# Performance work log

Hardware: AMD Instinct MI355X
Metric: run time of the kernel (lower is better)

## Reference

```python
import jax, jax.numpy as jnp
import numpy as np

EMBED = 1024
HEADS = 16
HEAD_DIM = EMBED // HEADS


def setup_inputs() -> dict:
    key = jax.random.key(0)
    k1, k2, k3 = jax.random.split(key, 3)
    B, T = 4, 2048
    query = jax.random.normal(k1, (B, T, EMBED), dtype=jnp.float32)
    # xavier-ish scaled weights
    in_proj_w = jax.random.normal(k2, (3 * EMBED, EMBED), dtype=jnp.float32) * (1.0 / np.sqrt(EMBED))
    in_proj_b = jnp.zeros((3 * EMBED,), dtype=jnp.float32)
    out_proj_w = jax.random.normal(k3, (EMBED, EMBED), dtype=jnp.float32) * (1.0 / np.sqrt(EMBED))
    out_proj_b = jnp.zeros((EMBED,), dtype=jnp.float32)
    return {"query": query, "in_proj_w": in_proj_w, "in_proj_b": in_proj_b,
            "out_proj_w": out_proj_w, "out_proj_b": out_proj_b}


def reference(query, in_proj_w, in_proj_b, out_proj_w, out_proj_b):
    # Self-attention (qkv_same path), batch_first=True, dropout=0 (eval).
    B, T, E = query.shape
    H, D = HEADS, HEAD_DIM
    scaling = D ** -0.5
    # fused QKV projection: [B,T,3E]
    qkv = jnp.einsum('bte,fe->btf', query, in_proj_w) + in_proj_b
    q, k, v = jnp.split(qkv, 3, axis=-1)
    q = q * scaling
    # reshape to [B,H,T,D]
    q = q.reshape(B, T, H, D).transpose(0, 2, 1, 3)
    k = k.reshape(B, T, H, D).transpose(0, 2, 1, 3)
    v = v.reshape(B, T, H, D).transpose(0, 2, 1, 3)
    scores = jnp.einsum('bhqd,bhkd->bhqk', q, k)
    attn = jax.nn.softmax(scores, axis=-1)
    ctx = jnp.einsum('bhqk,bhkd->bhqd', attn, v)  # [B,H,T,D]
    ctx = ctx.transpose(0, 2, 1, 3).reshape(B, T, E)
    out = jnp.einsum('bte,fe->btf', ctx, out_proj_w) + out_proj_b
    return out
```

## Files before the change

### kernel.cpp

```cpp
#include <hip/hip_runtime.h>
#include <math.h>

using bf16x8 = __attribute__((ext_vector_type(8))) short;
using f32x4  = __attribute__((ext_vector_type(4))) float;
using u16x8  = __attribute__((ext_vector_type(8))) unsigned short;
using u16x4  = __attribute__((ext_vector_type(4))) unsigned short;

constexpr int Bb = 4, Tt = 2048, Ee = 1024, Hh = 16;
constexpr int Mm = Bb * Tt;
constexpr int E3 = 3 * Ee;

__device__ __forceinline__ unsigned short f2bf(float f) {
  union { float f; unsigned int u; } c; c.f = f;
  unsigned int u = c.u;
  u += 0x7fffu + ((u >> 16) & 1u);
  return (unsigned short)(u >> 16);
}

__device__ __forceinline__ f32x4 mfma16(bf16x8 a, bf16x8 b, f32x4 c) {
  return __builtin_amdgcn_mfma_f32_16x16x32_bf16(a, b, c, 0, 0, 0);
}

__device__ __forceinline__ void gload_lds16(const unsigned short* g, unsigned short* l) {
  __builtin_amdgcn_global_load_lds(
      (const __attribute__((address_space(1))) unsigned int*)g,
      (__attribute__((address_space(3))) unsigned int*)l, 16, 0, 0);
}

__global__ void cvt_all(const float* __restrict__ q, const float* __restrict__ iw,
                        const float* __restrict__ ow, unsigned short* __restrict__ qb,
                        unsigned short* __restrict__ wib, unsigned short* __restrict__ wob) {
  constexpr int nQ = Mm * Ee / 8, nI = E3 * Ee / 8, nO = Ee * Ee / 8;
  int i = blockIdx.x * 256 + threadIdx.x;
  const float* in; unsigned short* out;
  if (i < nQ) { in = q; out = qb; }
  else if (i < nQ + nI) { in = iw; out = wib; i -= nQ; }
  else if (i < nQ + nI + nO) { in = ow; out = wob; i -= nQ + nI; }
  else return;
  const float4* p = (const float4*)in + (size_t)i * 2;
  const float4 a = p[0], b = p[1];
  u16x8 r = { f2bf(a.x), f2bf(a.y), f2bf(a.z), f2bf(a.w),
              f2bf(b.x), f2bf(b.y), f2bf(b.z), f2bf(b.w) };
  *(u16x8*)(out + (size_t)i * 8) = r;
}

template <bool OUT_BF16, bool QSCALE>
__global__ __launch_bounds__(256, 2)
void gemm_bt(const unsigned short* __restrict__ A, const unsigned short* __restrict__ Bw,
             const float* __restrict__ bias, void* __restrict__ Cout, int N, int K) {
  __shared__ alignas(16) unsigned short As[128 * 32];
  __shared__ alignas(16) unsigned short Bs[128 * 32];
  const int tid = threadIdx.x;
  const int wave = tid >> 6, lane = tid & 63;
  const int l15 = lane & 15, quad = lane >> 4;
  const int wr = wave >> 1, wc = wave & 1;
  const int row0 = blockIdx.y * 128, col0 = blockIdx.x * 128;
  const int srow = lane >> 2, sslot = lane & 3;

  f32x4 acc[4][4];
#pragma unroll
  for (int i = 0; i < 4; ++i)
#pragma unroll
    for (int j = 0; j < 4; ++j) acc[i][j] = f32x4{0.f, 0.f, 0.f, 0.f};

  for (int k0 = 0; k0 < K; k0 += 32) {
#pragma unroll
    for (int t = 0; t < 2; ++t) {
      const int rA = wave * 32 + t * 16 + srow;
      const int g = sslot ^ ((rA >> 1) & 3);
      gload_lds16(A  + (size_t)(row0 + rA) * K + k0 + g * 8, &As[(wave * 32 + t * 16) * 32]);
      gload_lds16(Bw + (size_t)(col0 + rA) * K + k0 + g * 8, &Bs[(wave * 32 + t * 16) * 32]);
    }
    __syncthreads();

    bf16x8 af[4], bfr[4];
#pragma unroll
    for (int mi = 0; mi < 4; ++mi) {
      const int m = wr * 64 + mi * 16 + l15;
      af[mi] = *(const bf16x8*)&As[m * 32 + (quad ^ ((m >> 1) & 3)) * 8];
    }
#pragma unroll
    for (int ni = 0; ni < 4; ++ni) {
      const int n = wc * 64 + ni * 16 + l15;
      bfr[ni] = *(const bf16x8*)&Bs[n * 32 + (quad ^ ((n >> 1) & 3)) * 8];
    }
#pragma unroll
    for (int mi = 0; mi < 4; ++mi)
#pragma unroll
      for (int ni = 0; ni < 4; ++ni) acc[mi][ni] = mfma16(af[mi], bfr[ni], acc[mi][ni]);
    __syncthreads();
  }

#pragma unroll
  for (int mi = 0; mi < 4; ++mi)
#pragma unroll
    for (int ni = 0; ni < 4; ++ni) {
      const int col = col0 + wc * 64 + ni * 16 + l15;
      const float bv = bias[col];
      const float scale = (QSCALE && col < 1024) ? 0.18033688f : 1.0f;
#pragma unroll
      for (int r = 0; r < 4; ++r) {
        const int row = row0 + wr * 64 + mi * 16 + quad * 4 + r;
        float v = (acc[mi][ni][r] + bv) * scale;
        if (OUT_BF16)
          ((unsigned short*)Cout)[(size_t)row * N + col] = f2bf(v);
        else
          ((float*)Cout)[(size_t)row * N + col] = v;
      }
    }
}

__global__ __launch_bounds__(256, 2)
void transpose_v(const unsigned short* __restrict__ qkv, unsigned short* __restrict__ vt) {
  __shared__ unsigned short L[128][66];
  const int tid = threadIdx.x;
  const int bh = blockIdx.x, b = bh >> 4, h = bh & 15;
  const int t0 = blockIdx.y * 128;
#pragma unroll
  for (int p = 0; p < 8; ++p) {
    const int tl = p * 16 + (tid >> 4);
    const int d = (tid & 15) * 4;
    *(u16x4*)&L[tl][d] = *(const u16x4*)(qkv + (size_t)(b * Tt + t0 + tl) * E3 + 2 * Ee + h * 64 + d);
  }
  __syncthreads();
#pragma unroll
  for (int p = 0; p < 8; ++p) {
    const int dw = (tid >> 5) * 8 + p;
    const int tw = (tid & 31) * 4;
    u16x4 w = { L[tw][dw], L[tw + 1][dw], L[tw + 2][dw], L[tw + 3][dw] };
    *(u16x4*)(vt + ((size_t)bh * 64 + dw) * Tt + t0 + tw) = w;
  }
}

__global__ __launch_bounds__(256, 2)
void attn_mfma6(const unsigned short* __restrict__ qkv,
                const unsigned short* __restrict__ vt,
                unsigned short* __restrict__ ctx) {
  __shared__ alignas(16) unsigned short Ps[4 * 4096];
  const int tid = threadIdx.x;
  const int wave = tid >> 6, lane = tid & 63;
  const int l15 = lane & 15, quad = lane >> 4;
  const int bh = blockIdx.x, b = bh >> 4, h = bh & 15;
  const int q0 = blockIdx.y * 256 + wave * 64;
  unsigned short* const ps = &Ps[wave * 4096];
  const int swz = l15 & 14;

  bf16x8 qa[4][2];
#pragma unroll
  for (int qi = 0; qi < 4; ++qi)
#pragma unroll
    for (int kf = 0; kf < 2; ++kf)
      qa[qi][kf] = *(const bf16x8*)(qkv +
          (size_t)(b * Tt + q0 + qi * 16 + l15) * E3 + h * 64 + kf * 32 + quad * 8);

  f32x4 o[4][4], ol[4];
#pragma unroll
  for (int qi = 0; qi < 4; ++qi) {
    ol[qi] = f32x4{0.f, 0.f, 0.f, 0.f};
#pragma unroll
    for (int di = 0; di < 4; ++di) o[qi][di] = f32x4{0.f, 0.f, 0.f, 0.f};
  }
  bf16x8 ones;
#pragma unroll
  for (int i = 0; i < 8; ++i) ones[i] = (short)0x3F80;

  const unsigned short* kp = qkv + (size_t)(b * Tt + l15) * E3 + Ee + h * 64 + quad * 8;
  const unsigned short* vp = vt + ((size_t)bh * 64 + l15) * Tt + quad * 8;

  bf16x8 kb[4][2], vb[4][2];
#pragma unroll
  for (int ki = 0; ki < 4; ++ki)
#pragma unroll
    for (int kf = 0; kf < 2; ++kf)
      kb[ki][kf] = *(const bf16x8*)(kp + (size_t)ki * 16 * E3 + kf * 32);
#pragma unroll
  for (int di = 0; di < 4; ++di)
#pragma unroll
    for (int kf = 0; kf < 2; ++kf)
      vb[di][kf] = *(const bf16x8*)(vp + di * 16 * Tt + kf * 32);
  kp += 64 * E3;
  vp += 64;

  f32x4 sp[4], sn[4];

  auto expwrite = [&](int slot) __attribute__((always_inline)) {
#pragma unroll
    for (int qi = 0; qi < 4; ++qi) {
      const float e0 = __builtin_amdgcn_exp2f(sp[qi][0]);
      const float e1 = __builtin_amdgcn_exp2f(sp[qi][1]);
      const float e2 = __builtin_amdgcn_exp2f(sp[qi][2]);
      const float e3 = __builtin_amdgcn_exp2f(sp[qi][3]);
      uint2 w;
      w.x = __builtin_amdgcn_perm(__float_as_uint(e1), __float_as_uint(e0), 0x07060302u);
      w.y = __builtin_amdgcn_perm(__float_as_uint(e3), __float_as_uint(e2), 0x07060302u);
      *(uint2*)(ps + (qi * 16 + l15) * 64 + (((slot * 4 + quad) ^ swz) << 2)) = w;
    }
  };
  auto Sstep = [&](int ki) __attribute__((always_inline)) {
#pragma unroll
    for (int qi = 0; qi < 4; ++qi) {
      sn[qi] = mfma16(kb[ki][0], qa[qi][0], f32x4{0.f, 0.f, 0.f, 0.f});
      sn[qi] = mfma16(kb[ki][1], qa[qi][1], sn[qi]);
    }
  };
  auto copy_sp = [&]() __attribute__((always_inline)) {
#pragma unroll
    for (int qi = 0; qi < 4; ++qi) sp[qi] = sn[qi];
  };
  auto pvstep = [&](bool reload_vb) __attribute__((always_inline)) {
#pragma unroll
    for (int qi = 0; qi < 4; ++qi) {
      bf16x8 pa0 = *(const bf16x8*)(ps + (qi * 16 + l15) * 64 + (((quad * 2) ^ swz) << 2));
      bf16x8 pa1 = *(const bf16x8*)(ps + (qi * 16 + l15) * 64 + (((8 + quad * 2) ^ swz) << 2));
      ol[qi] = mfma16(pa0, ones, ol[qi]);
      ol[qi] = mfma16(pa1, ones, ol[qi]);
#pragma unroll
      for (int di = 0; di < 4; ++di) {
        o[qi][di] = mfma16(pa0, vb[di][0], o[qi][di]);
        o[qi][di] = mfma16(pa1, vb[di][1], o[qi][di]);
      }
    }
    if (reload_vb) {
#pragma unroll
      for (int di = 0; di < 4; ++di)
#pragma unroll
        for (int kf = 0; kf < 2; ++kf)
          vb[di][kf] = *(const bf16x8*)(vp + di * 16 * Tt + kf * 32);
      vp += 64;
    }
  };

  Sstep(0); copy_sp();
  kb[0][0] = *(const bf16x8*)(kp);
  kb[0][1] = *(const bf16x8*)(kp + 32);

  for (int j = 0; j < 31; ++j) {
    expwrite(0);
    Sstep(1);
    kb[1][0] = *(const bf16x8*)(kp + (size_t)16 * E3);
    kb[1][1] = *(const bf16x8*)(kp + (size_t)16 * E3 + 32);
    copy_sp();
    expwrite(1);
    Sstep(2);
    kb[2][0] = *(const bf16x8*)(kp + (size_t)32 * E3);
    kb[2][1] = *(const bf16x8*)(kp + (size_t)32 * E3 + 32);
    copy_sp();
    expwrite(2);
    Sstep(3);
    kb[3][0] = *(const bf16x8*)(kp + (size_t)48 * E3);
    kb[3][1] = *(const bf16x8*)(kp + (size_t)48 * E3 + 32);
    kp += 64 * E3;
    copy_sp();
    expwrite(3);
    Sstep(0);
    if (j < 30) {
      kb[0][0] = *(const bf16x8*)(kp);
      kb[0][1] = *(const bf16x8*)(kp + 32);
    }
    copy_sp();
    pvstep(true);
  }
  expwrite(0); Sstep(1); copy_sp();
  expwrite(1); Sstep(2); copy_sp();
  expwrite(2); Sstep(3); copy_sp();
  expwrite(3);
  pvstep(false);

#pragma unroll
  for (int qi = 0; qi < 4; ++qi) {
    f32x4 inv;
#pragma unroll
    for (int r = 0; r < 4; ++r) inv[r] = 1.0f / ol[qi][r];
#pragma unroll
    for (int di = 0; di < 4; ++di)
#pragma unroll
      for (int r = 0; r < 4; ++r)
        ctx[(size_t)(b * Tt + q0 + qi * 16 + quad * 4 + r) * Ee + h * 64 + di * 16 + l15] =
            f2bf(o[qi][di][r] * inv[r]);
  }
}

extern "C" void kernel_launch(void* const* d_in, const int* in_sizes, int n_in,
                              void* d_out, int out_size, void* d_ws, size_t ws_size,
                              hipStream_t stream) {
  const float* query = (const float*)d_in[0];
  const float* in_w  = (const float*)d_in[1];
  const float* in_b  = (const float*)d_in[2];
  const float* out_w = (const float*)d_in[3];
  const float* out_b = (const float*)d_in[4];
  float* out = (float*)d_out;

  char* w = (char*)d_ws;
  unsigned short* qkvb = (unsigned short*)(w);
  unsigned short* ctxb = (unsigned short*)(w + 50331648);
  unsigned short* qb   = (unsigned short*)(w + 67108864);
  unsigned short* wib  = (unsigned short*)(w + 83886080);
  unsigned short* wob  = (unsigned short*)(w + 90177536);
  unsigned short* vtb  = (unsigned short*)(w + 92274688);

  cvt_all<<<6144, 256, 0, stream>>>(query, in_w, out_w, qb, wib, wob);
  gemm_bt<true, true><<<dim3(E3 / 128, Mm / 128), 256, 0, stream>>>(qb, wib, in_b, qkvb, E3, Ee);
  transpose_v<<<dim3(Bb * Hh, Tt / 128), 256, 0, stream>>>(qkvb, vtb);
  attn_mfma6<<<dim3(Bb * Hh, Tt / 256), 256, 0, stream>>>(qkvb, vtb, ctxb);
  gemm_bt<false, false><<<dim3(Ee / 128, Mm / 128), 256, 0, stream>>>(ctxb, wob, out_b, out, Ee, Ee);
}
```

Before: 313.0 us.

## Split attention key range across wave pairs and merge partial sums in LDS

Doubles the attention block to 512 threads so that each 64-query group is handled by two waves. Each wave processes half of the key sequence, so each wave runs half as many loop iterations. The second wave writes its partial output and row-sum to LDS, and the first wave adds them before normalizing and storing. This aims to raise the number of waves per CU and shorten each wave's serial loop. The costs are doubled LDS, an extra combine step with two barriers, and a tighter per-thread register budget under the new launch bounds, which could cause spills.

```diff
diff --git a/kernel.cpp b/kernel.cpp
--- a/kernel.cpp
+++ b/kernel.cpp
@@ -132,16 +132,18 @@
   }
 }
 
-__global__ __launch_bounds__(256, 2)
+__global__ __launch_bounds__(512, 2)
 void attn_mfma6(const unsigned short* __restrict__ qkv,
                 const unsigned short* __restrict__ vt,
                 unsigned short* __restrict__ ctx) {
-  __shared__ alignas(16) unsigned short Ps[4 * 4096];
+  __shared__ alignas(16) unsigned short Ps[8 * 4096];
+  __shared__ float olpart[4][64];
   const int tid = threadIdx.x;
   const int wave = tid >> 6, lane = tid & 63;
   const int l15 = lane & 15, quad = lane >> 4;
+  const int qgroup = wave >> 1, khalf = wave & 1;
   const int bh = blockIdx.x, b = bh >> 4, h = bh & 15;
-  const int q0 = blockIdx.y * 256 + wave * 64;
+  const int q0 = blockIdx.y * 256 + qgroup * 64;
   unsigned short* const ps = &Ps[wave * 4096];
   const int swz = l15 & 14;
 
@@ -164,8 +166,8 @@
 #pragma unroll
   for (int i = 0; i < 8; ++i) ones[i] = (short)0x3F80;
 
-  const unsigned short* kp = qkv + (size_t)(b * Tt + l15) * E3 + Ee + h * 64 + quad * 8;
-  const unsigned short* vp = vt + ((size_t)bh * 64 + l15) * Tt + quad * 8;
+  const unsigned short* kp = qkv + (size_t)(b * Tt + khalf * 1024 + l15) * E3 + Ee + h * 64 + quad * 8;
+  const unsigned short* vp = vt + ((size_t)bh * 64 + l15) * Tt + khalf * 1024 + quad * 8;
 
   bf16x8 kb[4][2], vb[4][2];
 #pragma unroll
@@ -234,7 +236,7 @@
   kb[0][0] = *(const bf16x8*)(kp);
   kb[0][1] = *(const bf16x8*)(kp + 32);
 
-  for (int j = 0; j < 31; ++j) {
+  for (int j = 0; j < 15; ++j) {
     expwrite(0);
     Sstep(1);
     kb[1][0] = *(const bf16x8*)(kp + (size_t)16 * E3);
@@ -253,7 +255,7 @@
     copy_sp();
     expwrite(3);
     Sstep(0);
-    if (j < 30) {
+    if (j < 14) {
       kb[0][0] = *(const bf16x8*)(kp);
       kb[0][1] = *(const bf16x8*)(kp + 32);
     }
@@ -266,17 +268,40 @@
   expwrite(3);
   pvstep(false);
 
-#pragma unroll
-  for (int qi = 0; qi < 4; ++qi) {
-    f32x4 inv;
-#pragma unroll
-    for (int r = 0; r < 4; ++r) inv[r] = 1.0f / ol[qi][r];
-#pragma unroll
-    for (int di = 0; di < 4; ++di)
+  __syncthreads();
+  float* const po = (float*)&Ps[(size_t)qgroup * 8192];
+  if (khalf) {
+#pragma unroll
+    for (int qi = 0; qi < 4; ++qi)
+#pragma unroll
+      for (int di = 0; di < 4; ++di)
+#pragma unroll
+        for (int r = 0; r < 4; ++r)
+          po[((qi * 4 + di) * 4 + r) * 64 + lane] = o[qi][di][r];
+    if (l15 == 0)
+#pragma unroll
+      for (int qi = 0; qi < 4; ++qi)
+#pragma unroll
+        for (int r = 0; r < 4; ++r)
+          olpart[qgroup][qi * 16 + quad * 4 + r] = ol[qi][r];
+  }
+  __syncthreads();
+  if (!khalf) {
+#pragma unroll
+    for (int qi = 0; qi < 4; ++qi) {
+      f32x4 inv;
 #pragma unroll
       for (int r = 0; r < 4; ++r)
-        ctx[(size_t)(b * Tt + q0 + qi * 16 + quad * 4 + r) * Ee + h * 64 + di * 16 + l15] =
-            f2bf(o[qi][di][r] * inv[r]);
+        inv[r] = 1.0f / (ol[qi][r] + olpart[qgroup][qi * 16 + quad * 4 + r]);
+#pragma unroll
+      for (int di = 0; di < 4; ++di)
+#pragma unroll
+        for (int r = 0; r < 4; ++r) {
+          const float v = o[qi][di][r] + po[((qi * 4 + di) * 4 + r) * 64 + lane];
+          ctx[(size_t)(b * Tt + q0 + qi * 16 + quad * 4 + r) * Ee + h * 64 + di * 16 + l15] =
+              f2bf(v * inv[r]);
+        }
+    }
   }
 }
 
@@ -301,6 +326,6 @@
   cvt_all<<<6144, 256, 0, stream>>>(query, in_w, out_w, qb, wib, wob);
   gemm_bt<true, true><<<dim3(E3 / 128, Mm / 128), 256, 0, stream>>>(qb, wib, in_b, qkvb, E3, Ee);
   transpose_v<<<dim3(Bb * Hh, Tt / 128), 256, 0, stream>>>(qkvb, vtb);
-  attn_mfma6<<<dim3(Bb * Hh, Tt / 256), 256, 0, stream>>>(qkvb, vtb, ctxb);
+  attn_mfma6<<<dim3(Bb * Hh, Tt / 256), 512, 0, stream>>>(qkvb, vtb, ctxb);
   gemm_bt<false, false><<<dim3(Ee / 128, Mm / 128), 256, 0, stream>>>(ctxb, wob, out_b, out, Ee, Ee);
 }
```

Result: slower. 319.6 us (+2.1%).

## Fuse V transpose into QKV GEMM epilogue and raise priority during PV MFMAs

Applied to the files above, without the earlier changes.

The QKV projection GEMM now writes the V slice directly in transposed [B,H,D,T] layout through an LDS staging tile, so the separate transpose_v kernel and its re-read of V from global memory are removed. V columns are no longer written to the qkv buffer, since attention reads V only from the transposed buffer. The attention kernel also raises wave priority around the PV MFMA block with s_setprio to favour the matrix pipe. The cost is extra LDS and two block-wide barriers in the GEMM epilogue for the V-tile blocks.

```diff
diff --git a/kernel.cpp b/kernel.cpp
--- a/kernel.cpp
+++ b/kernel.cpp
@@ -44,10 +44,11 @@
   *(u16x8*)(out + (size_t)i * 8) = r;
 }
 
-template <bool OUT_BF16, bool QSCALE>
+template <bool OUT_BF16, bool QSCALE, bool VT>
 __global__ __launch_bounds__(256, 2)
 void gemm_bt(const unsigned short* __restrict__ A, const unsigned short* __restrict__ Bw,
-             const float* __restrict__ bias, void* __restrict__ Cout, int N, int K) {
+             const float* __restrict__ bias, void* __restrict__ Cout,
+             unsigned short* __restrict__ vt, int N, int K) {
   __shared__ alignas(16) unsigned short As[128 * 32];
   __shared__ alignas(16) unsigned short Bs[128 * 32];
   const int tid = threadIdx.x;
@@ -91,6 +92,41 @@
     __syncthreads();
   }
 
+  if constexpr (VT) {
+    if (col0 >= 2048) {
+      __shared__ unsigned short Ct[64][136];
+      const int b  = row0 >> 11;
+      const int t0 = row0 & 2047;
+#pragma unroll
+      for (int hh = 0; hh < 2; ++hh) {
+        __syncthreads();
+        if (wc == hh) {
+#pragma unroll
+          for (int ni = 0; ni < 4; ++ni) {
+            const int d = ni * 16 + l15;
+            const float bv = bias[col0 + hh * 64 + d];
+#pragma unroll
+            for (int mi = 0; mi < 4; ++mi) {
+              const int t = wr * 64 + mi * 16 + quad * 4;
+              u16x4 wv;
+#pragma unroll
+              for (int r = 0; r < 4; ++r) wv[r] = f2bf(acc[mi][ni][r] + bv);
+              *(u16x4*)&Ct[d][t] = wv;
+            }
+          }
+        }
+        __syncthreads();
+        const int d = tid >> 2, tq = (tid & 3) * 32;
+        const int bh = b * 16 + ((col0 - 2048) >> 6) + hh;
+#pragma unroll
+        for (int s = 0; s < 4; ++s)
+          *(u16x8*)(vt + ((size_t)bh * 64 + d) * (size_t)Tt + t0 + tq + s * 8) =
+              *(const u16x8*)&Ct[d][tq + s * 8];
+      }
+      return;
+    }
+  }
+
 #pragma unroll
   for (int mi = 0; mi < 4; ++mi)
 #pragma unroll
@@ -108,28 +144,6 @@
           ((float*)Cout)[(size_t)row * N + col] = v;
       }
     }
-}
-
-__global__ __launch_bounds__(256, 2)
-void transpose_v(const unsigned short* __restrict__ qkv, unsigned short* __restrict__ vt) {
-  __shared__ unsigned short L[128][66];
-  const int tid = threadIdx.x;
-  const int bh = blockIdx.x, b = bh >> 4, h = bh & 15;
-  const int t0 = blockIdx.y * 128;
-#pragma unroll
-  for (int p = 0; p < 8; ++p) {
-    const int tl = p * 16 + (tid >> 4);
-    const int d = (tid & 15) * 4;
-    *(u16x4*)&L[tl][d] = *(const u16x4*)(qkv + (size_t)(b * Tt + t0 + tl) * E3 + 2 * Ee + h * 64 + d);
-  }
-  __syncthreads();
-#pragma unroll
-  for (int p = 0; p < 8; ++p) {
-    const int dw = (tid >> 5) * 8 + p;
-    const int tw = (tid & 31) * 4;
-    u16x4 w = { L[tw][dw], L[tw + 1][dw], L[tw + 2][dw], L[tw + 3][dw] };
-    *(u16x4*)(vt + ((size_t)bh * 64 + dw) * Tt + t0 + tw) = w;
-  }
 }
 
 __global__ __launch_bounds__(256, 2)
@@ -208,6 +222,7 @@
     for (int qi = 0; qi < 4; ++qi) sp[qi] = sn[qi];
   };
   auto pvstep = [&](bool reload_vb) __attribute__((always_inline)) {
+    __builtin_amdgcn_s_setprio(1);
 #pragma unroll
     for (int qi = 0; qi < 4; ++qi) {
       bf16x8 pa0 = *(const bf16x8*)(ps + (qi * 16 + l15) * 64 + (((quad * 2) ^ swz) << 2));
@@ -220,6 +235,7 @@
         o[qi][di] = mfma16(pa1, vb[di][1], o[qi][di]);
       }
     }
+    __builtin_amdgcn_s_setprio(0);
     if (reload_vb) {
 #pragma unroll
       for (int di = 0; di < 4; ++di)
@@ -299,8 +315,9 @@
   unsigned short* vtb  = (unsigned short*)(w + 92274688);
 
   cvt_all<<<6144, 256, 0, stream>>>(query, in_w, out_w, qb, wib, wob);
-  gemm_bt<true, true><<<dim3(E3 / 128, Mm / 128), 256, 0, stream>>>(qb, wib, in_b, qkvb, E3, Ee);
-  transpose_v<<<dim3(Bb * Hh, Tt / 128), 256, 0, stream>>>(qkvb, vtb);
+  gemm_bt<true, true, true><<<dim3(E3 / 128, Mm / 128), 256, 0, stream>>>(
+      qb, wib, in_b, qkvb, vtb, E3, Ee);
   attn_mfma6<<<dim3(Bb * Hh, Tt / 256), 256, 0, stream>>>(qkvb, vtb, ctxb);
-  gemm_bt<false, false><<<dim3(Ee / 128, Mm / 128), 256, 0, stream>>>(ctxb, wob, out_b, out, Ee, Ee);
-}
+  gemm_bt<false, false, false><<<dim3(Ee / 128, Mm / 128), 256, 0, stream>>>(
+      ctxb, wob, out_b, out, nullptr, Ee, Ee);
+}
```

Measured after the change: 308.7 us. No clear change (-1.4%).

## Replace QKV projection GEMM with 256x256 8-wave pipelined LDS kernel

Applied to the files above, without the earlier changes.

Adds a new 512-thread GEMM for the QKV projection that computes 256x256 output tiles. It streams A and B through a 4-slot LDS ring using direct global-to-LDS loads, with XOR swizzle, a block-index swizzle for cache locality, and interleaved barriers so MFMA quadrants overlap the next K-tile loads. It also raises wave priority around the MFMA bursts in both the new GEMM and the attention PV step. The goal is more data reuse per tile and better overlap of load latency with compute, at the cost of heavy register and LDS use (128 KB shared) and more complex synchronisation.

```diff
diff --git a/kernel.cpp b/kernel.cpp
--- a/kernel.cpp
+++ b/kernel.cpp
@@ -26,6 +26,11 @@
       (const __attribute__((address_space(1))) unsigned int*)g,
       (__attribute__((address_space(3))) unsigned int*)l, 16, 0, 0);
 }
+
+#define BAR()   __builtin_amdgcn_s_barrier()
+#define LGKM0() do { asm volatile("s_waitcnt lgkmcnt(0)" ::: "memory"); \
+                     __builtin_amdgcn_sched_barrier(0); } while (0)
+#define VMC(n)  asm volatile("s_waitcnt vmcnt(" #n ")" ::: "memory")
 
 __global__ void cvt_all(const float* __restrict__ q, const float* __restrict__ iw,
                         const float* __restrict__ ow, unsigned short* __restrict__ qb,
@@ -44,6 +49,148 @@
   *(u16x8*)(out + (size_t)i * 8) = r;
 }
 
+template <int MH, int NH>
+__device__ __forceinline__ void mmaQuad(f32x4 (&acc)[8][4], const bf16x8* af, const bf16x8* bf) {
+  __builtin_amdgcn_s_setprio(1);
+#pragma unroll
+  for (int i = 0; i < 4; ++i)
+#pragma unroll
+    for (int j = 0; j < 2; ++j) {
+      acc[MH * 4 + i][NH * 2 + j] = mfma16(af[i * 2 + 0], bf[j * 2 + 0], acc[MH * 4 + i][NH * 2 + j]);
+      acc[MH * 4 + i][NH * 2 + j] = mfma16(af[i * 2 + 1], bf[j * 2 + 1], acc[MH * 4 + i][NH * 2 + j]);
+    }
+  __builtin_amdgcn_s_setprio(0);
+}
+
+__global__ __launch_bounds__(512, 2)
+void gemm_bt8(const unsigned short* __restrict__ A, const unsigned short* __restrict__ Bw,
+              const float* __restrict__ bias, unsigned short* __restrict__ Cout,
+              int N, int K) {
+  __shared__ alignas(16) unsigned short lds8[8 * 8192];
+  const int tid = threadIdx.x;
+  const int wave = tid >> 6, lane = tid & 63;
+  const int l15 = lane & 15, quad = lane >> 4;
+  const int wm = wave >> 2, wn = wave & 3;
+  const int nt = K >> 6;
+
+  const int cpx = gridDim.x >> 3;
+  const int swz = (blockIdx.x & 7) * cpx + (blockIdx.x >> 3);
+  const int ntiles = N >> 8;
+  const int mtile = swz & 31, ntile = swz / 32;
+  (void)ntiles;
+  const int row0 = mtile << 8, col0 = ntile << 8;
+
+  int lrow[2], lcbh[2];
+#pragma unroll
+  for (int j = 0; j < 2; ++j) {
+    const int linoff = (j * 512 + tid) << 4;
+    const int logical = linoff ^ (((linoff >> 9) & 1) << 5);
+    lrow[j] = logical >> 7;
+    lcbh[j] = (logical & 127) >> 1;
+  }
+  unsigned int aoff[2][2], boff[2][2];
+#pragma unroll
+  for (int j = 0; j < 2; ++j) {
+    aoff[0][j] = (unsigned int)(row0 + lrow[j]) * K + lcbh[j];
+    aoff[1][j] = (unsigned int)(row0 + 128 + lrow[j]) * K + lcbh[j];
+    boff[0][j] = (unsigned int)(col0 + lrow[j]) * K + lcbh[j];
+    boff[1][j] = (unsigned int)(col0 + 128 + lrow[j]) * K + lcbh[j];
+  }
+  const int ldsW = wave * 512;
+
+  int aro[8], bro[4];
+#pragma unroll
+  for (int i = 0; i < 4; ++i)
+#pragma unroll
+    for (int kq = 0; kq < 2; ++kq) {
+      int lb = (i * 32 + wm * 16 + l15) * 128 + kq * 64 + quad * 16;
+      lb ^= ((lb >> 9) & 1) << 5;
+      aro[i * 2 + kq] = lb;
+    }
+#pragma unroll
+  for (int i = 0; i < 2; ++i)
+#pragma unroll
+    for (int kq = 0; kq < 2; ++kq) {
+      int lb = (i * 64 + wn * 16 + l15) * 128 + kq * 64 + quad * 16;
+      lb ^= ((lb >> 9) & 1) << 5;
+      bro[i * 2 + kq] = lb;
+    }
+
+  f32x4 acc[8][4];
+#pragma unroll
+  for (int i = 0; i < 8; ++i)
+#pragma unroll
+    for (int j = 0; j < 4; ++j) acc[i][j] = f32x4{0.f, 0.f, 0.f, 0.f};
+  bf16x8 af[8], bf0[4], bf1[4];
+
+  auto stageA = [&](int slot, int half, int kt) __attribute__((always_inline)) {
+#pragma unroll
+    for (int j = 0; j < 2; ++j)
+      gload_lds16(A + (size_t)aoff[half][j] + kt * 64,
+                  &lds8[slot * 8192 + j * 4096 + ldsW]);
+  };
+  auto stageB = [&](int slot, int half, int kt) __attribute__((always_inline)) {
+#pragma unroll
+    for (int j = 0; j < 2; ++j)
+      gload_lds16(Bw + (size_t)boff[half][j] + kt * 64,
+                  &lds8[(4 + slot) * 8192 + j * 4096 + ldsW]);
+  };
+  auto ldA = [&](int slot) __attribute__((always_inline)) {
+    const char* base = (const char*)lds8 + slot * 16384;
+#pragma unroll
+    for (int x = 0; x < 8; ++x) af[x] = *(const bf16x8*)(base + aro[x]);
+  };
+  auto ldB = [&](bf16x8* bf, int slot) __attribute__((always_inline)) {
+    const char* base = (const char*)lds8 + (4 + slot) * 16384;
+#pragma unroll
+    for (int x = 0; x < 4; ++x) bf[x] = *(const bf16x8*)(base + bro[x]);
+  };
+
+  stageA(0, 0, 0); stageA(1, 1, 0);
+  stageB(0, 0, 0); stageB(1, 1, 0);
+  stageA(2, 0, 1); stageB(3, 1, 1);
+  VMC(4); BAR();
+
+  for (int u = 0; u < nt; ++u) {
+    const int sae = (2 * u) & 3, sao = (2 * u + 1) & 3;
+    const int t1 = (u + 1 < nt) ? u + 1 : nt - 1;
+    const int t2 = (u + 2 < nt) ? u + 2 : nt - 1;
+    ldA(sae); ldB(bf0, sae);
+    stageA((2 * u + 3) & 3, 1, t1);
+    BAR(); LGKM0();
+    mmaQuad<0, 0>(acc, af, bf0);
+    VMC(2); BAR();
+    ldB(bf1, sao);
+    stageB((2 * u + 2) & 3, 0, t1);
+    BAR(); LGKM0();
+    mmaQuad<0, 1>(acc, af, bf1);
+    BAR();
+    ldA(sao);
+    stageA(sae, 0, t2);
+    BAR(); LGKM0();
+    mmaQuad<1, 1>(acc, af, bf1);
+    BAR();
+    stageB(sao, 1, t2);
+    BAR();
+    mmaQuad<1, 0>(acc, af, bf0);
+    VMC(4); BAR();
+  }
+
+#pragma unroll
+  for (int mi = 0; mi < 8; ++mi)
+#pragma unroll
+    for (int ni = 0; ni < 4; ++ni) {
+      const int col = col0 + ni * 64 + wn * 16 + l15;
+      const float bv = bias[col];
+      const float scale = (col < 1024) ? 0.18033688f : 1.0f;
+#pragma unroll
+      for (int r = 0; r < 4; ++r) {
+        const int row = row0 + mi * 32 + wm * 16 + quad * 4 + r;
+        Cout[(size_t)row * N + col] = f2bf((acc[mi][ni][r] + bv) * scale);
+      }
+    }
+}
+
 template <bool OUT_BF16, bool QSCALE>
 __global__ __launch_bounds__(256, 2)
 void gemm_bt(const unsigned short* __restrict__ A, const unsigned short* __restrict__ Bw,
@@ -208,6 +355,7 @@
     for (int qi = 0; qi < 4; ++qi) sp[qi] = sn[qi];
   };
   auto pvstep = [&](bool reload_vb) __attribute__((always_inline)) {
+    __builtin_amdgcn_s_setprio(1);
 #pragma unroll
     for (int qi = 0; qi < 4; ++qi) {
       bf16x8 pa0 = *(const bf16x8*)(ps + (qi * 16 + l15) * 64 + (((quad * 2) ^ swz) << 2));
@@ -220,6 +368,7 @@
         o[qi][di] = mfma16(pa1, vb[di][1], o[qi][di]);
       }
     }
+    __builtin_amdgcn_s_setprio(0);
     if (reload_vb) {
 #pragma unroll
       for (int di = 0; di < 4; ++di)
@@ -299,7 +448,7 @@
   unsigned short* vtb  = (unsigned short*)(w + 92274688);
 
   cvt_all<<<6144, 256, 0, stream>>>(query, in_w, out_w, qb, wib, wob);
-  gemm_bt<true, true><<<dim3(E3 / 128, Mm / 128), 256, 0, stream>>>(qb, wib, in_b, qkvb, E3, Ee);
+  gemm_bt8<<<dim3((E3 / 256) * (Mm / 256)), 512, 0, stream>>>(qb, wib, in_b, qkvb, E3, Ee);
   transpose_v<<<dim3(Bb * Hh, Tt / 128), 256, 0, stream>>>(qkvb, vtb);
   attn_mfma6<<<dim3(Bb * Hh, Tt / 256), 256, 0, stream>>>(qkvb, vtb, ctxb);
   gemm_bt<false, false><<<dim3(Ee / 128, Mm / 128), 256, 0, stream>>>(ctxb, wob, out_b, out, Ee, Ee);
```

Result: slower. 320.3 us (+2.4%).
